# Kernel optimization log

Measured on AMD Instinct MI355X. Metric: run time of the kernel, lower is better.

## Reference

```python
import jax, jax.numpy as jnp
import numpy as np

B, N, D = 1, 2048, 1024
H = 16
HD = D // H
MAX_REL = 100          # relative_positional_distance
NUM_EMB = 2 * MAX_REL - 1
NEG = 1e8


def _rel_pos_logits(q_pos, rel_emb):
    """Fairseq-style learned relative positional logits (unmasked).

    q_pos:   [L, B*H, hd]  (unscaled queries)
    rel_emb: [H, 2*MAX_REL-1, hd]
    returns: [B*H, L, L]
    """
    L = q_pos.shape[0]
    pad_len = max(L - MAX_REL, 0)
    start = max(MAX_REL - L, 0)
    # get_embeddings_for_query: pad to cover relative offsets -(L-1)..(L-1)
    padded = jnp.pad(rel_emb, ((0, 0), (pad_len, pad_len), (0, 0)))
    used = padded[:, start:start + 2 * L - 1, :]          # [H, 2L-1, hd]
    # calculate_positional_logits
    q4 = q_pos.reshape(L, -1, H, HD)                       # [L, B, H, hd]
    logits = jnp.einsum('lbhd,hmd->lbhm', q4, used)        # [L, B, H, 2L-1]
    logits = logits.reshape(L, -1, 2 * L - 1)              # [L, BH, 2L-1]
    if pad_len > 0:  # mask relative positions beyond max_relative_pos
        logits = logits.at[:, :, :pad_len].add(-NEG)
        logits = logits.at[:, :, -pad_len:].add(-NEG)
    # relative_to_absolute_indexing (unmasked skewing trick)
    bh = logits.shape[1]
    x = jnp.pad(logits, ((0, 0), (0, 0), (0, 1)))          # [L, BH, 2L]
    x = jnp.transpose(x, (1, 0, 2)).reshape(bh, L * 2 * L)
    x = jnp.pad(x, ((0, 0), (0, L - 1)))
    x = x.reshape(bh, L + 1, 2 * L - 1)
    return x[:, :L, L - 1:]                                # [BH, L, L]


def setup_inputs() -> dict:
    key = jax.random.key(0)
    ks = jax.random.split(key, 6)
    x = jax.random.normal(ks[0], (B, N, D), dtype=jnp.float32)
    qkv_w = jax.random.normal(ks[1], (3 * D, D), dtype=jnp.float32) * 0.02
    qkv_b = jnp.zeros((3 * D,), dtype=jnp.float32)
    proj_w = jax.random.normal(ks[2], (D, D), dtype=jnp.float32) * 0.02
    proj_b = jnp.zeros((D,), dtype=jnp.float32)
    rel_emb = jax.random.normal(ks[3], (H, NUM_EMB, HD), dtype=jnp.float32) * (HD ** -0.5)
    return {"x": x, "qkv_w": qkv_w, "qkv_b": qkv_b,
            "proj_w": proj_w, "proj_b": proj_b, "rel_emb": rel_emb}


def reference(x, qkv_w, qkv_b, proj_w, proj_b, rel_emb):
    b, n, d = x.shape
    qkv = x @ qkv_w.T + qkv_b                                # [B,N,3D]
    qkv = qkv.reshape(b, n, 3, H, HD).transpose(2, 0, 3, 1, 4)
    q, k, v = qkv[0], qkv[1], qkv[2]                          # [B,H,N,hd]
    scale = 1.0 / np.sqrt(HD).astype(np.float32)
    logits = jnp.einsum('bhqd,bhkd->bhqk', q, k) * scale      # [B,H,N,N]
    q_pos = jnp.transpose(q, (0, 2, 1, 3)).reshape(n, b * H, HD)
    pos = _rel_pos_logits(q_pos, rel_emb).reshape(b, H, n, n)
    probs = jax.nn.softmax(logits + pos, axis=-1)             # dropout off (eval)
    out = jnp.einsum('bhqk,bhkd->bhqd', probs, v)
    out = jnp.transpose(out, (0, 2, 1, 3)).reshape(b, n, d)
    return out @ proj_w.T + proj_b
```

## Files before the change

### kernel.cpp

```cpp
#include <hip/hip_runtime.h>
#include <hip/hip_bf16.h>

#define N_SEQ 2048
#define DMODEL 1024
#define NHEAD 16
#define HD 64
#define NREL 199

typedef __bf16 bf16x8 __attribute__((ext_vector_type(8)));
typedef float f32x4 __attribute__((ext_vector_type(4)));

__device__ __forceinline__ bf16x8 cvt8(float4 a, float4 b) {
    bf16x8 r;
    r[0] = (__bf16)a.x; r[1] = (__bf16)a.y; r[2] = (__bf16)a.z; r[3] = (__bf16)a.w;
    r[4] = (__bf16)b.x; r[5] = (__bf16)b.y; r[6] = (__bf16)b.z; r[7] = (__bf16)b.w;
    return r;
}

#define MFMA16(A, B, C) __builtin_amdgcn_mfma_f32_16x16x32_bf16(A, B, C, 0, 0, 0)

__device__ __forceinline__ void async_copy16(void* lds, const void* g) {
    __builtin_amdgcn_global_load_lds(
        (__attribute__((address_space(1))) unsigned int*)g,
        (__attribute__((address_space(3))) unsigned int*)lds, 16, 0, 0);
}

__global__ __launch_bounds__(256) void cvt3(
    const float* __restrict__ a, __bf16* __restrict__ ao, int na,
    const float* __restrict__ b, __bf16* __restrict__ bo, int nb,
    const float* __restrict__ c, __bf16* __restrict__ co)
{
    int i = (blockIdx.x * blockDim.x + threadIdx.x) * 8;
    const float* src; __bf16* dst;
    if (i < na)              { src = a + i;            dst = ao + i; }
    else if (i - na < nb)    { src = b + (i - na);     dst = bo + (i - na); }
    else                     { src = c + (i - na - nb); dst = co + (i - na - nb); }
    float4 f0 = ((const float4*)src)[0];
    float4 f1 = ((const float4*)src)[1];
    *(bf16x8*)dst = cvt8(f0, f1);
}

template<int BM, int BN, bool OUT_BF16>
__global__ __launch_bounds__(256) void gemm_db(
    const __bf16* __restrict__ A,
    const __bf16* __restrict__ W,
    const float* __restrict__ bias,
    void* __restrict__ Cout,
    int lda, int Nc, int K, int ldc)
{
    constexpr int RT = BM + BN;
    constexpr int WM = BM / 2, WN = BN / 2;
    constexpr int MI = WM / 16, NI = WN / 16;
    constexpr int CHUNKS = RT / 4 / 8;

    __shared__ __bf16 s[2][RT][64];

    const int tid  = threadIdx.x;
    const int wid  = tid >> 6;
    const int lane = tid & 63;
    const int quad = lane >> 4;
    const int l15  = lane & 15;
    const int wm   = (wid >> 1) * WM;
    const int wn   = (wid & 1) * WN;
    const int bm   = blockIdx.y * BM;
    const int bn   = blockIdx.x * BN;

    const int lrow = lane >> 3;
    const int lcb  = ((lane & 7) ^ lrow) * 8;

    f32x4 acc[MI][NI] = {};

    auto stage = [&](int buf, int k0) {
        #pragma unroll
        for (int c = 0; c < CHUNKS; c++) {
            const int r0 = wid * (RT / 4) + c * 8;
            const __bf16* src = (r0 < BM)
                ? A + (size_t)(bm + r0 + lrow) * lda + k0 + lcb
                : W + (size_t)(bn + (r0 - BM) + lrow) * K + k0 + lcb;
            async_copy16(&s[buf][r0][0], src);
        }
    };

    stage(0, 0);
    int cur = 0;
    for (int k0 = 0; k0 < K; k0 += 64) {
        __syncthreads();
        if (k0 + 64 < K) stage(cur ^ 1, k0 + 64);

        #pragma unroll
        for (int half = 0; half < 2; half++) {
            bf16x8 af[MI], bfr[NI];
            #pragma unroll
            for (int mi = 0; mi < MI; mi++) {
                int ar = wm + mi * 16 + l15;
                af[mi] = *(const bf16x8*)&s[cur][ar][((quad + 4 * half) ^ (ar & 7)) * 8];
            }
            #pragma unroll
            for (int ni = 0; ni < NI; ni++) {
                int br = BM + wn + ni * 16 + l15;
                bfr[ni] = *(const bf16x8*)&s[cur][br][((quad + 4 * half) ^ (br & 7)) * 8];
            }
            #pragma unroll
            for (int mi = 0; mi < MI; mi++)
                #pragma unroll
                for (int ni = 0; ni < NI; ni++)
                    acc[mi][ni] = MFMA16(af[mi], bfr[ni], acc[mi][ni]);
        }
        cur ^= 1;
    }

    #pragma unroll
    for (int ni = 0; ni < NI; ni++) {
        int col = bn + wn + ni * 16 + l15;
        float bv = bias[col];
        #pragma unroll
        for (int mi = 0; mi < MI; mi++)
            #pragma unroll
            for (int ri = 0; ri < 4; ri++) {
                int row = bm + wm + mi * 16 + quad * 4 + ri;
                float v = acc[mi][ni][ri] + bv;
                if (OUT_BF16)
                    reinterpret_cast<__bf16*>(Cout)[(size_t)row * ldc + col] = (__bf16)v;
                else
                    reinterpret_cast<float*>(Cout)[(size_t)row * ldc + col] = v;
            }
    }
}

__global__ __launch_bounds__(256) void attn_band_mfma(
    __hip_bfloat16* __restrict__ qkv,
    const float* __restrict__ rel_emb)
{
    __shared__ __align__(16) char smem[53248];
    __bf16 (*q_s)[72]   = (__bf16(*)[72])smem;
    __bf16 (*p_s)[72]   = (__bf16(*)[72])smem;
    __bf16 (*P_s)[200]  = (__bf16(*)[200])(smem + 9216);
    __bf16 (*relc)[72]  = (__bf16(*)[72])(smem + 34816);
    __bf16 (*k_s)[72]   = (__bf16(*)[72])(smem + 34816);
    __bf16 (*v_s)[72]   = (__bf16(*)[72])(smem + 34816 + 9216);

    const int tid  = threadIdx.x;
    const int wid  = tid >> 6;
    const int lane = tid & 63;
    const int quad = lane >> 4;
    const int l15  = lane & 15;
    const int h    = blockIdx.x >> 5;
    const int q0   = (blockIdx.x & 31) * 64;
    const int srow = tid >> 2;
    const int sq   = (tid & 3) * 16;

    const int j_lo   = (q0 - 99 > 0) ? (q0 - 99) : 0;
    const int j_hi   = (q0 + 162 < N_SEQ - 1) ? (q0 + 162) : (N_SEQ - 1);
    const int ntiles = (j_hi - j_lo + 64) >> 6;

    uint4 kr0, kr1, vr0, vr1;
    {
        int jr = j_lo + srow; if (jr > N_SEQ - 1) jr = N_SEQ - 1;
        const uint4* ks = (const uint4*)(qkv + (size_t)jr * 3072 + 1024 + h * HD + sq);
        kr0 = ks[0]; kr1 = ks[1];
        const uint4* vs = (const uint4*)(qkv + (size_t)jr * 3072 + 2048 + h * HD + sq);
        vr0 = vs[0]; vr1 = vs[1];
    }

    {
        const __hip_bfloat16* src = qkv + (size_t)(q0 + srow) * 3072 + h * HD + sq;
        uint4 u0 = ((const uint4*)src)[0];
        uint4 u1 = ((const uint4*)src)[1];
        *(uint4*)&q_s[srow][sq]     = u0;
        *(uint4*)&q_s[srow][sq + 8] = u1;
    }
    for (int idx = tid; idx < 112 * 4; idx += 256) {
        int er = idx >> 2, ec = (idx & 3) * 16;
        const float4* s = (const float4*)(rel_emb + ((size_t)h * NREL + er) * HD + ec);
        float4 f0 = s[0], f1 = s[1], f2 = s[2], f3 = s[3];
        *(bf16x8*)&relc[er][ec]     = cvt8(f0, f1);
        *(bf16x8*)&relc[er][ec + 8] = cvt8(f2, f3);
    }
    __syncthreads();

    const bf16x8 aq0 = *(const bf16x8*)&q_s[wid * 16 + l15][quad * 8];
    const bf16x8 aq1 = *(const bf16x8*)&q_s[wid * 16 + l15][quad * 8 + 32];

    #pragma unroll
    for (int t = 0; t < 7; t++) {
        f32x4 pacc = {};
        bf16x8 b0 = *(const bf16x8*)&relc[t * 16 + l15][quad * 8];
        bf16x8 b1 = *(const bf16x8*)&relc[t * 16 + l15][quad * 8 + 32];
        pacc = MFMA16(aq0, b0, pacc);
        pacc = MFMA16(aq1, b1, pacc);
        #pragma unroll
        for (int ri = 0; ri < 4; ri++)
            P_s[wid * 16 + quad * 4 + ri][t * 16 + l15] = (__bf16)pacc[ri];
    }
    __syncthreads();

    for (int idx = tid; idx < 96 * 4; idx += 256) {
        int er = 112 + (idx >> 2); if (er > NREL - 1) er = NREL - 1;
        int ec = (idx & 3) * 16;
        const float4* s = (const float4*)(rel_emb + ((size_t)h * NREL + er) * HD + ec);
        float4 f0 = s[0], f1 = s[1], f2 = s[2], f3 = s[3];
        *(bf16x8*)&relc[idx >> 2][ec]     = cvt8(f0, f1);
        *(bf16x8*)&relc[idx >> 2][ec + 8] = cvt8(f2, f3);
    }
    __syncthreads();

    #pragma unroll
    for (int t = 7; t < 13; t++) {
        f32x4 pacc = {};
        bf16x8 b0 = *(const bf16x8*)&relc[t * 16 + l15 - 112][quad * 8];
        bf16x8 b1 = *(const bf16x8*)&relc[t * 16 + l15 - 112][quad * 8 + 32];
        pacc = MFMA16(aq0, b0, pacc);
        pacc = MFMA16(aq1, b1, pacc);
        #pragma unroll
        for (int ri = 0; ri < 4; ri++) {
            int col = t * 16 + l15;
            if (col < NREL)
                P_s[wid * 16 + quad * 4 + ri][col] = (__bf16)pacc[ri];
        }
    }

    bf16x8 bones;
    {
        __bf16 o = (l15 == 0) ? (__bf16)1.0f : (__bf16)0.0f;
        #pragma unroll
        for (int i = 0; i < 8; i++) bones[i] = o;
    }

    f32x4 O[4] = {};
    f32x4 Osum = {};

    for (int t = 0; t < ntiles; t++) {
        __syncthreads();

        *(uint4*)&k_s[srow][sq]     = kr0;
        *(uint4*)&k_s[srow][sq + 8] = kr1;
        {
            __bf16 vtmp[16];
            *(uint4*)&vtmp[0] = vr0; *(uint4*)&vtmp[8] = vr1;
            #pragma unroll
            for (int i = 0; i < 16; i++) v_s[sq + i][srow] = vtmp[i];
        }
        __syncthreads();

        if (t + 1 < ntiles) {
            int jr = j_lo + (t + 1) * 64 + srow; if (jr > N_SEQ - 1) jr = N_SEQ - 1;
            const uint4* ks = (const uint4*)(qkv + (size_t)jr * 3072 + 1024 + h * HD + sq);
            kr0 = ks[0]; kr1 = ks[1];
            const uint4* vs = (const uint4*)(qkv + (size_t)jr * 3072 + 2048 + h * HD + sq);
            vr0 = vs[0]; vr1 = vs[1];
        }

        const int j0 = j_lo + t * 64;

        f32x4 S[4] = {};
        #pragma unroll
        for (int nt = 0; nt < 4; nt++) {
            bf16x8 b0 = *(const bf16x8*)&k_s[nt * 16 + l15][quad * 8];
            bf16x8 b1 = *(const bf16x8*)&k_s[nt * 16 + l15][quad * 8 + 32];
            S[nt] = MFMA16(aq0, b0, S[nt]);
            S[nt] = MFMA16(aq1, b1, S[nt]);
        }

        #pragma unroll
        for (int nt = 0; nt < 4; nt++) {
            int jg = j0 + nt * 16 + l15;
            #pragma unroll
            for (int ri = 0; ri < 4; ri++) {
                int r_loc = wid * 16 + quad * 4 + ri;
                int e = jg - (q0 + r_loc) + 99;
                float v = -3.0e38f;
                if ((unsigned)e < (unsigned)NREL && jg < N_SEQ)
                    v = S[nt][ri] * 0.125f + (float)P_s[r_loc][e];
                float p = __expf(v);
                p_s[r_loc][nt * 16 + l15] = (__bf16)p;
            }
        }

        bf16x8 ap0 = *(const bf16x8*)&p_s[wid * 16 + l15][quad * 8];
        bf16x8 ap1 = *(const bf16x8*)&p_s[wid * 16 + l15][quad * 8 + 32];
        #pragma unroll
        for (int nt = 0; nt < 4; nt++) {
            bf16x8 b0 = *(const bf16x8*)&v_s[nt * 16 + l15][quad * 8];
            bf16x8 b1 = *(const bf16x8*)&v_s[nt * 16 + l15][quad * 8 + 32];
            O[nt] = MFMA16(ap0, b0, O[nt]);
            O[nt] = MFMA16(ap1, b1, O[nt]);
        }
        Osum = MFMA16(ap0, bones, Osum);
        Osum = MFMA16(ap1, bones, Osum);
    }

    #pragma unroll
    for (int ri = 0; ri < 4; ri++) {
        float s = __shfl(Osum[ri], (lane & 48), 64);
        float inv = 1.0f / s;
        #pragma unroll
        for (int nt = 0; nt < 4; nt++) {
            int r = q0 + wid * 16 + quad * 4 + ri;
            qkv[(size_t)r * 3072 + h * HD + nt * 16 + l15] =
                __float2bfloat16(O[nt][ri] * inv);
        }
    }
}

extern "C" void kernel_launch(void* const* d_in, const int* in_sizes, int n_in,
                              void* d_out, int out_size, void* d_ws, size_t ws_size,
                              hipStream_t stream)
{
    (void)out_size; (void)ws_size; (void)n_in;

    const float *x = nullptr, *qkv_w = nullptr, *qkv_b = nullptr;
    const float *proj_w = nullptr, *proj_b = nullptr, *rel = nullptr;
    for (int i = 0; i < 6; i++) {
        switch (in_sizes[i]) {
            case 2097152: x      = (const float*)d_in[i]; break;
            case 3145728: qkv_w  = (const float*)d_in[i]; break;
            case 3072:    qkv_b  = (const float*)d_in[i]; break;
            case 1048576: proj_w = (const float*)d_in[i]; break;
            case 1024:    proj_b = (const float*)d_in[i]; break;
            case 203776:  rel    = (const float*)d_in[i]; break;
            default: break;
        }
    }

    char* ws = (char*)d_ws;
    __hip_bfloat16* qkv = (__hip_bfloat16*)ws;
    __bf16* xb  = (__bf16*)(ws + 12582912);
    __bf16* wb  = (__bf16*)(ws + 16777216);
    __bf16* pwb = (__bf16*)(ws + 23068672);
    float* out = (float*)d_out;

    cvt3<<<dim3(6291456 / 8 / 256), 256, 0, stream>>>(
        x, xb, 2097152, qkv_w, wb, 3145728, proj_w, pwb);
    gemm_db<128, 96, true><<<dim3(3072 / 96, N_SEQ / 128), 256, 0, stream>>>(
        xb, wb, qkv_b, (void*)qkv, DMODEL, 3072, DMODEL, 3072);
    attn_band_mfma<<<dim3(NHEAD * (N_SEQ / 64)), 256, 0, stream>>>(qkv, rel);
    gemm_db<64, 64, false><<<dim3(DMODEL / 64, N_SEQ / 64), 256, 0, stream>>>(
        (const __bf16*)qkv, pwb, proj_b, (void*)out, 3072, DMODEL, DMODEL, DMODEL);
}
```

Measured before the change: 126.1 us.

## Double-buffer K/V tiles, skip out-of-band tiles, fold proj weight cast into attention

The attention kernel now keeps two LDS buffers for K/V, so the next tile is staged while the current one is computed, and each iteration needs one barrier instead of two. j_lo is aligned to 64, and each wave skips tiles that lie wholly outside its 16-row relative-position band. MFMA sections are wrapped in s_setprio. The proj_w fp32-to-bf16 cast moves out of cvt3 into 16 extra blocks of the attention launch, which shortens the cast kernel. The cost is more dynamic shared memory (70 KB), which may lower occupancy, plus a one-time function attribute call.

```diff
diff --git a/kernel.cpp b/kernel.cpp
--- a/kernel.cpp
+++ b/kernel.cpp
@@ -129,15 +129,30 @@
 
 __global__ __launch_bounds__(256) void attn_band_mfma(
     __hip_bfloat16* __restrict__ qkv,
-    const float* __restrict__ rel_emb)
+    const float* __restrict__ rel_emb,
+    const float* __restrict__ pw,
+    __bf16* __restrict__ pwb)
 {
-    __shared__ __align__(16) char smem[53248];
-    __bf16 (*q_s)[72]   = (__bf16(*)[72])smem;
-    __bf16 (*p_s)[72]   = (__bf16(*)[72])smem;
-    __bf16 (*P_s)[200]  = (__bf16(*)[200])(smem + 9216);
-    __bf16 (*relc)[72]  = (__bf16(*)[72])(smem + 34816);
-    __bf16 (*k_s)[72]   = (__bf16(*)[72])(smem + 34816);
-    __bf16 (*v_s)[72]   = (__bf16(*)[72])(smem + 34816 + 9216);
+    if (blockIdx.x >= NHEAD * 32) {
+        const int b = blockIdx.x - NHEAD * 32;
+        const int base = b * 65536 + threadIdx.x * 8;
+        #pragma unroll 4
+        for (int it = 0; it < 32; it++) {
+            int i = base + it * 2048;
+            float4 f0 = ((const float4*)(pw + i))[0];
+            float4 f1 = ((const float4*)(pw + i))[1];
+            *(bf16x8*)(pwb + i) = cvt8(f0, f1);
+        }
+        return;
+    }
+
+    extern __shared__ __align__(16) char smem[];
+    __bf16 (*q_s)[72]      = (__bf16(*)[72])smem;
+    __bf16 (*p_s)[72]      = (__bf16(*)[72])smem;
+    __bf16 (*P_s)[200]     = (__bf16(*)[200])(smem + 9216);
+    __bf16 (*relc)[72]     = (__bf16(*)[72])(smem + 34816);
+    __bf16 (*k_s)[64][72]  = (__bf16(*)[64][72])(smem + 34816);
+    __bf16 (*v_s)[64][72]  = (__bf16(*)[64][72])(smem + 34816 + 18432);
 
     const int tid  = threadIdx.x;
     const int wid  = tid >> 6;
@@ -149,7 +164,8 @@
     const int srow = tid >> 2;
     const int sq   = (tid & 3) * 16;
 
-    const int j_lo   = (q0 - 99 > 0) ? (q0 - 99) : 0;
+    int j_lo = q0 - 99;
+    if (j_lo < 0) j_lo = 0; else j_lo &= ~63;
     const int j_hi   = (q0 + 162 < N_SEQ - 1) ? (q0 + 162) : (N_SEQ - 1);
     const int ntiles = (j_hi - j_lo + 64) >> 6;
 
@@ -228,65 +244,90 @@
 
     f32x4 O[4] = {};
     f32x4 Osum = {};
+    const int r0w = q0 + wid * 16;
+
+    __syncthreads();
+    *(uint4*)&k_s[0][srow][sq]     = kr0;
+    *(uint4*)&k_s[0][srow][sq + 8] = kr1;
+    {
+        __bf16 vtmp[16];
+        *(uint4*)&vtmp[0] = vr0; *(uint4*)&vtmp[8] = vr1;
+        #pragma unroll
+        for (int i = 0; i < 16; i++) v_s[0][sq + i][srow] = vtmp[i];
+    }
+    if (1 < ntiles) {
+        int jr = j_lo + 64 + srow; if (jr > N_SEQ - 1) jr = N_SEQ - 1;
+        const uint4* ks = (const uint4*)(qkv + (size_t)jr * 3072 + 1024 + h * HD + sq);
+        kr0 = ks[0]; kr1 = ks[1];
+        const uint4* vs = (const uint4*)(qkv + (size_t)jr * 3072 + 2048 + h * HD + sq);
+        vr0 = vs[0]; vr1 = vs[1];
+    }
+    __syncthreads();
 
     for (int t = 0; t < ntiles; t++) {
-        __syncthreads();
-
-        *(uint4*)&k_s[srow][sq]     = kr0;
-        *(uint4*)&k_s[srow][sq + 8] = kr1;
-        {
-            __bf16 vtmp[16];
-            *(uint4*)&vtmp[0] = vr0; *(uint4*)&vtmp[8] = vr1;
-            #pragma unroll
-            for (int i = 0; i < 16; i++) v_s[sq + i][srow] = vtmp[i];
-        }
-        __syncthreads();
+        const int cur = t & 1;
+        const int j0  = j_lo + t * 64;
+
+        if (j0 <= r0w + 114 && j0 + 63 >= r0w - 99) {
+            f32x4 S[4] = {};
+            __builtin_amdgcn_s_setprio(1);
+            #pragma unroll
+            for (int nt = 0; nt < 4; nt++) {
+                bf16x8 b0 = *(const bf16x8*)&k_s[cur][nt * 16 + l15][quad * 8];
+                bf16x8 b1 = *(const bf16x8*)&k_s[cur][nt * 16 + l15][quad * 8 + 32];
+                S[nt] = MFMA16(aq0, b0, S[nt]);
+                S[nt] = MFMA16(aq1, b1, S[nt]);
+            }
+            __builtin_amdgcn_s_setprio(0);
+
+            #pragma unroll
+            for (int nt = 0; nt < 4; nt++) {
+                int jg = j0 + nt * 16 + l15;
+                #pragma unroll
+                for (int ri = 0; ri < 4; ri++) {
+                    int r_loc = wid * 16 + quad * 4 + ri;
+                    int e = jg - (q0 + r_loc) + 99;
+                    float v = -3.0e38f;
+                    if ((unsigned)e < (unsigned)NREL && jg < N_SEQ)
+                        v = S[nt][ri] * 0.125f + (float)P_s[r_loc][e];
+                    float p = __expf(v);
+                    p_s[r_loc][nt * 16 + l15] = (__bf16)p;
+                }
+            }
+
+            bf16x8 ap0 = *(const bf16x8*)&p_s[wid * 16 + l15][quad * 8];
+            bf16x8 ap1 = *(const bf16x8*)&p_s[wid * 16 + l15][quad * 8 + 32];
+            __builtin_amdgcn_s_setprio(1);
+            #pragma unroll
+            for (int nt = 0; nt < 4; nt++) {
+                bf16x8 b0 = *(const bf16x8*)&v_s[cur][nt * 16 + l15][quad * 8];
+                bf16x8 b1 = *(const bf16x8*)&v_s[cur][nt * 16 + l15][quad * 8 + 32];
+                O[nt] = MFMA16(ap0, b0, O[nt]);
+                O[nt] = MFMA16(ap1, b1, O[nt]);
+            }
+            Osum = MFMA16(ap0, bones, Osum);
+            Osum = MFMA16(ap1, bones, Osum);
+            __builtin_amdgcn_s_setprio(0);
+        }
 
         if (t + 1 < ntiles) {
-            int jr = j_lo + (t + 1) * 64 + srow; if (jr > N_SEQ - 1) jr = N_SEQ - 1;
-            const uint4* ks = (const uint4*)(qkv + (size_t)jr * 3072 + 1024 + h * HD + sq);
-            kr0 = ks[0]; kr1 = ks[1];
-            const uint4* vs = (const uint4*)(qkv + (size_t)jr * 3072 + 2048 + h * HD + sq);
-            vr0 = vs[0]; vr1 = vs[1];
-        }
-
-        const int j0 = j_lo + t * 64;
-
-        f32x4 S[4] = {};
-        #pragma unroll
-        for (int nt = 0; nt < 4; nt++) {
-            bf16x8 b0 = *(const bf16x8*)&k_s[nt * 16 + l15][quad * 8];
-            bf16x8 b1 = *(const bf16x8*)&k_s[nt * 16 + l15][quad * 8 + 32];
-            S[nt] = MFMA16(aq0, b0, S[nt]);
-            S[nt] = MFMA16(aq1, b1, S[nt]);
-        }
-
-        #pragma unroll
-        for (int nt = 0; nt < 4; nt++) {
-            int jg = j0 + nt * 16 + l15;
-            #pragma unroll
-            for (int ri = 0; ri < 4; ri++) {
-                int r_loc = wid * 16 + quad * 4 + ri;
-                int e = jg - (q0 + r_loc) + 99;
-                float v = -3.0e38f;
-                if ((unsigned)e < (unsigned)NREL && jg < N_SEQ)
-                    v = S[nt][ri] * 0.125f + (float)P_s[r_loc][e];
-                float p = __expf(v);
-                p_s[r_loc][nt * 16 + l15] = (__bf16)p;
-            }
-        }
-
-        bf16x8 ap0 = *(const bf16x8*)&p_s[wid * 16 + l15][quad * 8];
-        bf16x8 ap1 = *(const bf16x8*)&p_s[wid * 16 + l15][quad * 8 + 32];
-        #pragma unroll
-        for (int nt = 0; nt < 4; nt++) {
-            bf16x8 b0 = *(const bf16x8*)&v_s[nt * 16 + l15][quad * 8];
-            bf16x8 b1 = *(const bf16x8*)&v_s[nt * 16 + l15][quad * 8 + 32];
-            O[nt] = MFMA16(ap0, b0, O[nt]);
-            O[nt] = MFMA16(ap1, b1, O[nt]);
-        }
-        Osum = MFMA16(ap0, bones, Osum);
-        Osum = MFMA16(ap1, bones, Osum);
+            *(uint4*)&k_s[cur ^ 1][srow][sq]     = kr0;
+            *(uint4*)&k_s[cur ^ 1][srow][sq + 8] = kr1;
+            {
+                __bf16 vtmp[16];
+                *(uint4*)&vtmp[0] = vr0; *(uint4*)&vtmp[8] = vr1;
+                #pragma unroll
+                for (int i = 0; i < 16; i++) v_s[cur ^ 1][sq + i][srow] = vtmp[i];
+            }
+            if (t + 2 < ntiles) {
+                int jr = j_lo + (t + 2) * 64 + srow; if (jr > N_SEQ - 1) jr = N_SEQ - 1;
+                const uint4* ks = (const uint4*)(qkv + (size_t)jr * 3072 + 1024 + h * HD + sq);
+                kr0 = ks[0]; kr1 = ks[1];
+                const uint4* vs = (const uint4*)(qkv + (size_t)jr * 3072 + 2048 + h * HD + sq);
+                vr0 = vs[0]; vr1 = vs[1];
+            }
+            __syncthreads();
+        }
     }
 
     #pragma unroll
@@ -329,11 +370,19 @@
     __bf16* pwb = (__bf16*)(ws + 23068672);
     float* out = (float*)d_out;
 
-    cvt3<<<dim3(6291456 / 8 / 256), 256, 0, stream>>>(
+    static bool attr_set = false;
+    if (!attr_set) {
+        hipFuncSetAttribute(reinterpret_cast<const void*>(attn_band_mfma),
+                            hipFuncAttributeMaxDynamicSharedMemorySize, 71680);
+        attr_set = true;
+    }
+
+    cvt3<<<dim3((2097152 + 3145728) / 8 / 256), 256, 0, stream>>>(
         x, xb, 2097152, qkv_w, wb, 3145728, proj_w, pwb);
     gemm_db<128, 96, true><<<dim3(3072 / 96, N_SEQ / 128), 256, 0, stream>>>(
         xb, wb, qkv_b, (void*)qkv, DMODEL, 3072, DMODEL, 3072);
-    attn_band_mfma<<<dim3(NHEAD * (N_SEQ / 64)), 256, 0, stream>>>(qkv, rel);
+    attn_band_mfma<<<dim3(NHEAD * (N_SEQ / 64) + 16), 256, 71680, stream>>>(
+        qkv, rel, proj_w, pwb);
     gemm_db<64, 64, false><<<dim3(DMODEL / 64, N_SEQ / 64), 256, 0, stream>>>(
         (const __bf16*)qkv, pwb, proj_b, (void*)out, 3072, DMODEL, DMODEL, DMODEL);
 }
```

Result: no change. 127.9 us (+1.4%).

## Fuse all stages into one cooperative persistent kernel with grid syncs

Applied to the files above, without the earlier changes.

Merges the conversion, QKV GEMM, banded attention and output projection into a single cooperative kernel of 512 blocks, separated by grid-wide barriers. The aim is to remove the launch gaps and tail effects between the four kernels. It also raises wave priority around the MFMA sections in attention. In exchange every stage runs on a fixed 512-block grid with 2 blocks per CU, and grid syncs add their own barrier cost. The old four-launch path remains only as a fallback if the cooperative launch fails.

```diff
diff --git a/kernel.cpp b/kernel.cpp
--- a/kernel.cpp
+++ b/kernel.cpp
@@ -1,5 +1,8 @@
 #include <hip/hip_runtime.h>
 #include <hip/hip_bf16.h>
+#include <hip/hip_cooperative_groups.h>
+
+namespace cg = cooperative_groups;
 
 #define N_SEQ 2048
 #define DMODEL 1024
@@ -25,45 +28,50 @@
         (__attribute__((address_space(3))) unsigned int*)lds, 16, 0, 0);
 }
 
-__global__ __launch_bounds__(256) void cvt3(
-    const float* __restrict__ a, __bf16* __restrict__ ao, int na,
-    const float* __restrict__ b, __bf16* __restrict__ bo, int nb,
-    const float* __restrict__ c, __bf16* __restrict__ co)
-{
-    int i = (blockIdx.x * blockDim.x + threadIdx.x) * 8;
-    const float* src; __bf16* dst;
-    if (i < na)              { src = a + i;            dst = ao + i; }
-    else if (i - na < nb)    { src = b + (i - na);     dst = bo + (i - na); }
-    else                     { src = c + (i - na - nb); dst = co + (i - na - nb); }
-    float4 f0 = ((const float4*)src)[0];
-    float4 f1 = ((const float4*)src)[1];
-    *(bf16x8*)dst = cvt8(f0, f1);
+
+__device__ __forceinline__ void cvt_phase(
+    int gid,
+    const float* __restrict__ x,  __bf16* __restrict__ xb,
+    const float* __restrict__ qw, __bf16* __restrict__ wb,
+    const float* __restrict__ pw, __bf16* __restrict__ pwb)
+{
+    #pragma unroll
+    for (int it = 0; it < 6; it++) {
+        int i = (gid + it * 131072) * 8;
+        const float* src; __bf16* dst;
+        if (i < 2097152)      { src = x  + i;             dst = xb  + i; }
+        else if (i < 5242880) { src = qw + (i - 2097152); dst = wb  + (i - 2097152); }
+        else                  { src = pw + (i - 5242880); dst = pwb + (i - 5242880); }
+        float4 f0 = ((const float4*)src)[0];
+        float4 f1 = ((const float4*)src)[1];
+        *(bf16x8*)dst = cvt8(f0, f1);
+    }
 }
 
 template<int BM, int BN, bool OUT_BF16>
-__global__ __launch_bounds__(256) void gemm_db(
+__device__ __forceinline__ void gemm_phase(
+    char* smem_,
     const __bf16* __restrict__ A,
     const __bf16* __restrict__ W,
     const float* __restrict__ bias,
     void* __restrict__ Cout,
-    int lda, int Nc, int K, int ldc)
+    int lda, int K, int ldc, int bx, int by, int tid)
 {
     constexpr int RT = BM + BN;
     constexpr int WM = BM / 2, WN = BN / 2;
     constexpr int MI = WM / 16, NI = WN / 16;
     constexpr int CHUNKS = RT / 4 / 8;
 
-    __shared__ __bf16 s[2][RT][64];
-
-    const int tid  = threadIdx.x;
+    __bf16 (*s)[RT][64] = (__bf16 (*)[RT][64])smem_;
+
     const int wid  = tid >> 6;
     const int lane = tid & 63;
     const int quad = lane >> 4;
     const int l15  = lane & 15;
     const int wm   = (wid >> 1) * WM;
     const int wn   = (wid & 1) * WN;
-    const int bm   = blockIdx.y * BM;
-    const int bn   = blockIdx.x * BN;
+    const int bm   = by * BM;
+    const int bn   = bx * BN;
 
     const int lrow = lane >> 3;
     const int lcb  = ((lane & 7) ^ lrow) * 8;
@@ -77,7 +85,7 @@
             const __bf16* src = (r0 < BM)
                 ? A + (size_t)(bm + r0 + lrow) * lda + k0 + lcb
                 : W + (size_t)(bn + (r0 - BM) + lrow) * K + k0 + lcb;
-            async_copy16(&s[buf][r0][0], src);
+            async_copy16(&s[buf][r0 + lrow - lrow][0], src);
         }
     };
 
@@ -127,11 +135,12 @@
     }
 }
 
-__global__ __launch_bounds__(256) void attn_band_mfma(
+__device__ __forceinline__ void attn_phase(
+    char* smem,
     __hip_bfloat16* __restrict__ qkv,
-    const float* __restrict__ rel_emb)
-{
-    __shared__ __align__(16) char smem[53248];
+    const float* __restrict__ rel_emb,
+    int bid, int tid)
+{
     __bf16 (*q_s)[72]   = (__bf16(*)[72])smem;
     __bf16 (*p_s)[72]   = (__bf16(*)[72])smem;
     __bf16 (*P_s)[200]  = (__bf16(*)[200])(smem + 9216);
@@ -139,13 +148,12 @@
     __bf16 (*k_s)[72]   = (__bf16(*)[72])(smem + 34816);
     __bf16 (*v_s)[72]   = (__bf16(*)[72])(smem + 34816 + 9216);
 
-    const int tid  = threadIdx.x;
     const int wid  = tid >> 6;
     const int lane = tid & 63;
     const int quad = lane >> 4;
     const int l15  = lane & 15;
-    const int h    = blockIdx.x >> 5;
-    const int q0   = (blockIdx.x & 31) * 64;
+    const int h    = bid >> 5;
+    const int q0   = (bid & 31) * 64;
     const int srow = tid >> 2;
     const int sq   = (tid & 3) * 16;
 
@@ -253,6 +261,7 @@
         const int j0 = j_lo + t * 64;
 
         f32x4 S[4] = {};
+        __builtin_amdgcn_s_setprio(1);
         #pragma unroll
         for (int nt = 0; nt < 4; nt++) {
             bf16x8 b0 = *(const bf16x8*)&k_s[nt * 16 + l15][quad * 8];
@@ -260,6 +269,7 @@
             S[nt] = MFMA16(aq0, b0, S[nt]);
             S[nt] = MFMA16(aq1, b1, S[nt]);
         }
+        __builtin_amdgcn_s_setprio(0);
 
         #pragma unroll
         for (int nt = 0; nt < 4; nt++) {
@@ -278,6 +288,7 @@
 
         bf16x8 ap0 = *(const bf16x8*)&p_s[wid * 16 + l15][quad * 8];
         bf16x8 ap1 = *(const bf16x8*)&p_s[wid * 16 + l15][quad * 8 + 32];
+        __builtin_amdgcn_s_setprio(1);
         #pragma unroll
         for (int nt = 0; nt < 4; nt++) {
             bf16x8 b0 = *(const bf16x8*)&v_s[nt * 16 + l15][quad * 8];
@@ -287,6 +298,7 @@
         }
         Osum = MFMA16(ap0, bones, Osum);
         Osum = MFMA16(ap1, bones, Osum);
+        __builtin_amdgcn_s_setprio(0);
     }
 
     #pragma unroll
@@ -300,6 +312,59 @@
                 __float2bfloat16(O[nt][ri] * inv);
         }
     }
+}
+
+__global__ __launch_bounds__(256, 2) void mega(
+    const float* x, const float* qkv_w, const float* qkv_b,
+    const float* proj_w, const float* proj_b, const float* rel_emb,
+    __hip_bfloat16* qkv, __bf16* xb, __bf16* wb, __bf16* pwb, float* out)
+{
+    extern __shared__ __align__(16) char smem[];
+    const int bid = blockIdx.x;
+    const int tid = threadIdx.x;
+
+    cvt_phase(bid * 256 + tid, x, xb, qkv_w, wb, proj_w, pwb);
+
+    __threadfence();
+    cg::this_grid().sync();
+
+    gemm_phase<128, 96, true>(smem, xb, wb, qkv_b, (void*)qkv,
+                              DMODEL, DMODEL, 3072, bid & 31, bid >> 5, tid);
+
+    __threadfence();
+    cg::this_grid().sync();
+
+    attn_phase(smem, qkv, rel_emb, bid, tid);
+
+    __threadfence();
+    cg::this_grid().sync();
+
+    gemm_phase<64, 64, false>(smem, (const __bf16*)qkv, pwb, proj_b, (void*)out,
+                              3072, DMODEL, DMODEL, bid & 15, bid >> 4, tid);
+}
+
+__global__ __launch_bounds__(256) void cvt_k(
+    const float* x, __bf16* xb, const float* qw, __bf16* wb,
+    const float* pw, __bf16* pwb)
+{
+    cvt_phase(blockIdx.x * 256 + threadIdx.x, x, xb, qw, wb, pw, pwb);
+}
+
+template<int BM, int BN, bool OUT_BF16>
+__global__ __launch_bounds__(256) void gemm_k(
+    const __bf16* A, const __bf16* W, const float* bias, void* C,
+    int lda, int K, int ldc)
+{
+    __shared__ __align__(16) char smem[2 * (BM + BN) * 64 * 2];
+    gemm_phase<BM, BN, OUT_BF16>(smem, A, W, bias, C, lda, K, ldc,
+                                 blockIdx.x, blockIdx.y, threadIdx.x);
+}
+
+__global__ __launch_bounds__(256) void attn_k(
+    __hip_bfloat16* qkv, const float* rel_emb)
+{
+    __shared__ __align__(16) char smem[53248];
+    attn_phase(smem, qkv, rel_emb, blockIdx.x, threadIdx.x);
 }
 
 extern "C" void kernel_launch(void* const* d_in, const int* in_sizes, int n_in,
@@ -329,11 +394,27 @@
     __bf16* pwb = (__bf16*)(ws + 23068672);
     float* out = (float*)d_out;
 
-    cvt3<<<dim3(6291456 / 8 / 256), 256, 0, stream>>>(
-        x, xb, 2097152, qkv_w, wb, 3145728, proj_w, pwb);
-    gemm_db<128, 96, true><<<dim3(3072 / 96, N_SEQ / 128), 256, 0, stream>>>(
-        xb, wb, qkv_b, (void*)qkv, DMODEL, 3072, DMODEL, 3072);
-    attn_band_mfma<<<dim3(NHEAD * (N_SEQ / 64)), 256, 0, stream>>>(qkv, rel);
-    gemm_db<64, 64, false><<<dim3(DMODEL / 64, N_SEQ / 64), 256, 0, stream>>>(
-        (const __bf16*)qkv, pwb, proj_b, (void*)out, 3072, DMODEL, DMODEL, DMODEL);
-}
+    static bool attr_set = false;
+    if (!attr_set) {
+        hipFuncSetAttribute(reinterpret_cast<const void*>(mega),
+                            hipFuncAttributeMaxDynamicSharedMemorySize, 57344);
+        attr_set = true;
+    }
+
+    void* args[] = {
+        (void*)&x, (void*)&qkv_w, (void*)&qkv_b, (void*)&proj_w, (void*)&proj_b,
+        (void*)&rel, (void*)&qkv, (void*)&xb, (void*)&wb, (void*)&pwb, (void*)&out
+    };
+    hipError_t e = hipLaunchCooperativeKernel(
+        reinterpret_cast<const void*>(mega), dim3(512), dim3(256),
+        args, 57344, stream);
+
+    if (e != hipSuccess) {
+        cvt_k<<<512, 256, 0, stream>>>(x, xb, qkv_w, wb, proj_w, pwb);
+        gemm_k<128, 96, true><<<dim3(32, 16), 256, 0, stream>>>(
+            xb, wb, qkv_b, (void*)qkv, DMODEL, DMODEL, 3072);
+        attn_k<<<512, 256, 0, stream>>>(qkv, rel);
+        gemm_k<64, 64, false><<<dim3(16, 32), 256, 0, stream>>>(
+            (const __bf16*)qkv, pwb, proj_b, (void*)out, 3072, DMODEL, DMODEL);
+    }
+}
```

Result: slower. 471.5 us (+273.9%).
